# Kernel optimization log

Hardware: AMD Instinct MI355X
Metric: run time of the kernel (lower is better)

## Reference

```python
import jax, jax.numpy as jnp
import numpy as np
from jax import lax

D_MODEL = 1024
KERNEL = 7
EPS = 1e-8


def setup_inputs() -> dict:
    key = jax.random.key(0)
    ks = jax.random.split(key, 8)
    B, T, D = 4, 4096, D_MODEL
    x = jax.random.normal(ks[0], (B, T, D), dtype=jnp.float32)
    # rotary tables [T, D/2]
    pos = jnp.arange(T, dtype=jnp.float32)[:, None]
    inv_freq = 1.0 / (10000.0 ** (jnp.arange(D // 2, dtype=jnp.float32) / (D // 2)))
    ang = pos * inv_freq[None, :]
    sin = jnp.sin(ang)
    cos = jnp.cos(ang)
    # params
    W_proj = jax.random.normal(ks[1], (D, 2 * D), dtype=jnp.float32) * (1.0 / np.sqrt(D))
    b_proj = jnp.zeros((2 * D,), dtype=jnp.float32)
    dw_kernel = jax.random.normal(ks[2], (KERNEL, 1, D), dtype=jnp.float32) * 0.1  # [K,1,C] WIO depthwise
    dw_bias = jnp.zeros((D,), dtype=jnp.float32)
    gamma = jnp.ones((D,), dtype=jnp.float32)
    return {"x": x, "sin": sin, "cos": cos, "W_proj": W_proj, "b_proj": b_proj,
            "dw_kernel": dw_kernel, "dw_bias": dw_bias, "gamma": gamma}


def reference(x, sin, cos, W_proj, b_proj, dw_kernel, dw_bias, gamma):
    D = D_MODEL
    proj = jnp.einsum('btd,df->btf', x, W_proj) + b_proj          # [B,T,2D]
    x_a, x_b = proj[..., :D], proj[..., D:]
    # interleaved rotary: even/odd pairs
    x1 = x_a[..., 0::2]                                            # [B,T,D/2]
    x2 = x_a[..., 1::2]
    c = cos[None, :, :]
    s = sin[None, :, :]
    r1 = x1 * c - x2 * s
    r2 = x1 * s + x2 * c
    x_rot = jnp.stack([r1, r2], axis=-1).reshape(x_a.shape)        # re-interleave
    # depthwise conv1d, SAME padding
    conv = lax.conv_general_dilated(
        x_rot, dw_kernel, window_strides=(1,), padding='SAME',
        dimension_numbers=('NWC', 'WIO', 'NWC'), feature_group_count=D) + dw_bias
    act = conv * jax.nn.sigmoid(conv)                              # swish
    gated = act * jax.nn.sigmoid(x_b)
    rms = jnp.sqrt(jnp.mean(jnp.square(gated), axis=-1, keepdims=True) + EPS)
    return gamma * (gated / rms)
```

## Files before the change

kernel.cpp:

```cpp
#include <hip/hip_runtime.h>
#include <stdint.h>

#define D_MODEL 1024
#define T_LEN   4096
#define B_SZ    4
#define NROWS   (B_SZ * T_LEN)
#define NPROJ   (2 * D_MODEL)
#define CHUNK   16

#define BM 256
#define BN 256
#define BK 64
#define NT (D_MODEL / BK)

typedef __attribute__((ext_vector_type(8))) __bf16 bf16x8;
typedef __attribute__((ext_vector_type(4))) float  f32x4;

using as1_void = __attribute__((address_space(1))) void;
using as3_void = __attribute__((address_space(3))) void;

__device__ inline float bf2f(unsigned short u) {
    union { unsigned int i; float f; } v; v.i = ((unsigned int)u) << 16; return v.f;
}
__device__ inline unsigned short f2bf(float f) {
    union { float f; unsigned int i; } v; v.f = f;
    return (unsigned short)((v.i + 0x7fffu + ((v.i >> 16) & 1u)) >> 16);
}
__device__ inline float sigmoidf(float x) { return 1.0f / (1.0f + __expf(-x)); }

__global__ __launch_bounds__(256) void k_cvt(const float* __restrict__ x,
                                             unsigned short* __restrict__ xb,
                                             const float* __restrict__ W,
                                             unsigned short* __restrict__ wt) {
    __shared__ unsigned short tile[32][33];
    int bid = blockIdx.x;
    if (bid < (NROWS * D_MODEL) / (256 * 4)) {
        int i = (bid * 256 + threadIdx.x) * 4;
        float4 v = *reinterpret_cast<const float4*>(x + i);
        ushort4 o;
        o.x = f2bf(v.x); o.y = f2bf(v.y); o.z = f2bf(v.z); o.w = f2bf(v.w);
        *reinterpret_cast<ushort4*>(xb + i) = o;
    } else {
        bid -= (NROWS * D_MODEL) / (256 * 4);
        int n0 = (bid & 63) * 32, k0 = (bid >> 6) * 32;
        int c = threadIdx.x & 31, r = threadIdx.x >> 5;
        #pragma unroll
        for (int i = 0; i < 4; i++) {
            int kk = r + i * 8;
            tile[kk][c] = f2bf(W[(uint64_t)(k0 + kk) * NPROJ + n0 + c]);
        }
        __syncthreads();
        #pragma unroll
        for (int i = 0; i < 4; i++) {
            int nn = r + i * 8;
            wt[(uint64_t)(n0 + nn) * D_MODEL + k0 + c] = tile[c][nn];
        }
    }
}

__global__ __launch_bounds__(512, 2) void k_gemm(const unsigned short* __restrict__ xb,
                                                 const unsigned short* __restrict__ wt,
                                                 const float* __restrict__ bias,
                                                 unsigned short* __restrict__ projb) {
    __shared__ __align__(16) unsigned short As[2 * BM * BK];
    __shared__ __align__(16) unsigned short Bs[2 * BM * BK];

    const int tid  = threadIdx.x;
    const int lane = tid & 63;
    const int w    = tid >> 6;
    const int wm   = w >> 2;
    const int wn   = w & 3;

    const int bid = blockIdx.x;
    const int wg  = (bid & 7) * 64 + (bid >> 3);
    const int n0  = (wg >> 6) * BN;
    const int m0  = (wg & 63) * BM;

    const int srow = tid >> 3;
    const int scol = ((tid & 7) ^ (srow & 7)) * 8;
    const int fr   = lane & 15;
    const int fq   = lane >> 4;

    f32x4 acc[8][4] = {};

    auto STAGE = [&](int buf, int ks) {
        #pragma unroll
        for (int i = 0; i < 4; ++i) {
            const unsigned short* ga = xb + (uint64_t)(m0 + i * 64 + srow) * D_MODEL + ks + scol;
            __builtin_amdgcn_global_load_lds((as1_void*)(void*)ga,
                (as3_void*)(void*)&As[buf * (BM * BK) + i * 4096 + w * 512], 16, 0, 0);
        }
        #pragma unroll
        for (int i = 0; i < 4; ++i) {
            const unsigned short* gb = wt + (uint64_t)(n0 + i * 64 + srow) * D_MODEL + ks + scol;
            __builtin_amdgcn_global_load_lds((as1_void*)(void*)gb,
                (as3_void*)(void*)&Bs[buf * (BM * BK) + i * 4096 + w * 512], 16, 0, 0);
        }
    };

    STAGE(0, 0);
    __syncthreads();

    for (int t = 0; t < NT; ++t) {
        const int cur = t & 1;
        if (t + 1 < NT) STAGE(1 - cur, (t + 1) * BK);

        const unsigned short* Ab = &As[cur * (BM * BK)];
        const unsigned short* Bb = &Bs[cur * (BM * BK)];
        #pragma unroll
        for (int kk = 0; kk < BK; kk += 32) {
            const int slot = (kk >> 3) + fq;
            bf16x8 b[4];
            #pragma unroll
            for (int n = 0; n < 4; n++) {
                const int rb = wn * 64 + n * 16 + fr;
                b[n] = *reinterpret_cast<const bf16x8*>(&Bb[rb * 64 + ((slot ^ (fr & 7)) * 8)]);
            }
            #pragma unroll
            for (int m = 0; m < 8; m++) {
                const int ra = wm * 128 + m * 16 + fr;
                bf16x8 a = *reinterpret_cast<const bf16x8*>(&Ab[ra * 64 + ((slot ^ (fr & 7)) * 8)]);
                #pragma unroll
                for (int n = 0; n < 4; n++)
                    acc[m][n] = __builtin_amdgcn_mfma_f32_16x16x32_bf16(a, b[n], acc[m][n], 0, 0, 0);
            }
        }
        __syncthreads();
    }

    #pragma unroll
    for (int m = 0; m < 8; m++) {
        const int grow = m0 + wm * 128 + m * 16 + fq * 4;
        #pragma unroll
        for (int n = 0; n < 4; n++) {
            const int gcol = n0 + wn * 64 + n * 16 + fr;
            const float bv = bias[gcol];
            #pragma unroll
            for (int r = 0; r < 4; r++) {
                projb[(uint64_t)(grow + r) * NPROJ + gcol] = f2bf(acc[m][n][r] + bv);
            }
        }
    }
}

__global__ __launch_bounds__(512) void k_post(const unsigned short* __restrict__ projb,
                                              const float* __restrict__ kw,
                                              const float* __restrict__ dwb,
                                              const float* __restrict__ gamma,
                                              float* __restrict__ out) {
    const int blk  = blockIdx.x;
    const int b    = blk / (T_LEN / CHUNK);
    const int t0   = (blk % (T_LEN / CHUNK)) * CHUNK;
    const int c    = threadIdx.x;
    const int d0   = c * 2;
    const uint64_t bbase = (uint64_t)b * T_LEN;

    const float invf = exp2f((float)c * (-13.287712379549449f / 512.0f));

    float kwv[7][2];
    #pragma unroll
    for (int j = 0; j < 7; j++) {
        kwv[j][0] = kw[j * D_MODEL + d0];
        kwv[j][1] = kw[j * D_MODEL + d0 + 1];
    }
    const float bv0 = dwb[d0], bv1 = dwb[d0 + 1];
    const float gm0 = gamma[d0], gm1 = gamma[d0 + 1];

    __shared__ float partial[CHUNK][8];
    __shared__ float invr[CHUNK];

    auto load_rope = [&](int tj, float& o0, float& o1) {
        if ((unsigned)tj < (unsigned)T_LEN) {
            ushort2 u = *reinterpret_cast<const ushort2*>(projb + (bbase + tj) * NPROJ + d0);
            float sv, cv;
            __sincosf((float)tj * invf, &sv, &cv);
            float x0 = bf2f(u.x), x1 = bf2f(u.y);
            o0 = x0 * cv - x1 * sv;
            o1 = x0 * sv + x1 * cv;
        } else { o0 = 0.f; o1 = 0.f; }
    };

    float rg[6][2];
    #pragma unroll
    for (int j = 0; j < 6; j++) load_rope(t0 - 3 + j, rg[j][0], rg[j][1]);

    float ga[CHUNK], gb[CHUNK];

    #pragma unroll
    for (int r = 0; r < CHUNK; ++r) {
        float nx0, nx1;
        load_rope(t0 + r + 3, nx0, nx1);
        ushort2 xbv = *reinterpret_cast<const ushort2*>(
            projb + (bbase + t0 + r) * NPROJ + D_MODEL + d0);

        float acc0 = rg[0][0] * kwv[0][0] + rg[1][0] * kwv[1][0] + rg[2][0] * kwv[2][0]
                   + rg[3][0] * kwv[3][0] + rg[4][0] * kwv[4][0] + rg[5][0] * kwv[5][0]
                   + nx0 * kwv[6][0] + bv0;
        float acc1 = rg[0][1] * kwv[0][1] + rg[1][1] * kwv[1][1] + rg[2][1] * kwv[2][1]
                   + rg[3][1] * kwv[3][1] + rg[4][1] * kwv[4][1] + rg[5][1] * kwv[5][1]
                   + nx1 * kwv[6][1] + bv1;

        float a0 = acc0 * sigmoidf(acc0);
        float a1 = acc1 * sigmoidf(acc1);
        float g0 = a0 * sigmoidf(bf2f(xbv.x));
        float g1 = a1 * sigmoidf(bf2f(xbv.y));
        ga[r] = g0; gb[r] = g1;

        float ssq = g0 * g0 + g1 * g1;
        #pragma unroll
        for (int off = 32; off; off >>= 1) ssq += __shfl_down(ssq, off);
        if ((c & 63) == 0) partial[r][c >> 6] = ssq;

        #pragma unroll
        for (int j = 0; j < 5; j++) { rg[j][0] = rg[j + 1][0]; rg[j][1] = rg[j + 1][1]; }
        rg[5][0] = nx0; rg[5][1] = nx1;
    }

    __syncthreads();
    if (c < CHUNK) {
        float s = partial[c][0] + partial[c][1] + partial[c][2] + partial[c][3]
                + partial[c][4] + partial[c][5] + partial[c][6] + partial[c][7];
        invr[c] = 1.0f / sqrtf(s * (1.0f / (float)D_MODEL) + 1e-8f);
    }
    __syncthreads();

    #pragma unroll
    for (int r = 0; r < CHUNK; ++r) {
        const float iv = invr[r];
        float2 o;
        o.x = ga[r] * iv * gm0;
        o.y = gb[r] * iv * gm1;
        *reinterpret_cast<float2*>(out + (bbase + t0 + r) * D_MODEL + d0) = o;
    }
}

extern "C" void kernel_launch(void* const* d_in, const int* in_sizes, int n_in,
                              void* d_out, int out_size, void* d_ws, size_t ws_size,
                              hipStream_t stream) {
    const float* x     = (const float*)d_in[0];
    const float* sinp  = (const float*)d_in[1];
    const float* cosp  = (const float*)d_in[2];
    const float* W     = (const float*)d_in[3];
    const float* bproj = (const float*)d_in[4];
    const float* dwk   = (const float*)d_in[5];
    const float* dwb   = (const float*)d_in[6];
    const float* gamma = (const float*)d_in[7];
    float* out = (float*)d_out;
    (void)sinp; (void)cosp;

    unsigned short* xb    = (unsigned short*)d_ws;
    unsigned short* wt    = xb + (size_t)NROWS * D_MODEL;
    unsigned short* projb = wt + (size_t)NPROJ * D_MODEL;

    const int cvt_x_blocks = (NROWS * D_MODEL) / (256 * 4);
    const int cvt_w_blocks = (NPROJ / 32) * (D_MODEL / 32);
    k_cvt<<<cvt_x_blocks + cvt_w_blocks, 256, 0, stream>>>(x, xb, W, wt);
    k_gemm<<<(NPROJ / BN) * (NROWS / BM), 512, 0, stream>>>(xb, wt, bproj, projb);
    k_post<<<B_SZ * (T_LEN / CHUNK), 512, 0, stream>>>(projb, dwk, dwb, gamma, out);
}
```

Baseline: 147.6 us.

## Batch post-kernel loads, use recurrence for rotary angles, widen conversion stores

The post kernel now issues all conv-tap and gate loads up front (clamped addresses) before any computation, halves CHUNK to 8 to shrink per-thread register arrays and double the block count, and replaces per-row sincos calls with a rotation recurrence. The x conversion kernel handles 8 elements per thread with 16-byte stores. The goal is better memory-level parallelism in the post kernel and fewer transcendental ops. The cost is more redundant halo loads per chunk, and the recurrence may slowly lose precision across rows.

```diff
diff --git a/kernel.cpp b/kernel.cpp
--- a/kernel.cpp
+++ b/kernel.cpp
@@ -6,7 +6,7 @@
 #define B_SZ    4
 #define NROWS   (B_SZ * T_LEN)
 #define NPROJ   (2 * D_MODEL)
-#define CHUNK   16
+#define CHUNK   8
 
 #define BM 256
 #define BN 256
@@ -26,22 +26,30 @@
     union { float f; unsigned int i; } v; v.f = f;
     return (unsigned short)((v.i + 0x7fffu + ((v.i >> 16) & 1u)) >> 16);
 }
+__device__ inline unsigned int f2bf2(float lo, float hi) {
+    return (unsigned int)f2bf(lo) | ((unsigned int)f2bf(hi) << 16);
+}
 __device__ inline float sigmoidf(float x) { return 1.0f / (1.0f + __expf(-x)); }
 
+#define CVT_X_BLOCKS ((NROWS * D_MODEL) / (256 * 8))
 __global__ __launch_bounds__(256) void k_cvt(const float* __restrict__ x,
                                              unsigned short* __restrict__ xb,
                                              const float* __restrict__ W,
                                              unsigned short* __restrict__ wt) {
     __shared__ unsigned short tile[32][33];
     int bid = blockIdx.x;
-    if (bid < (NROWS * D_MODEL) / (256 * 4)) {
-        int i = (bid * 256 + threadIdx.x) * 4;
-        float4 v = *reinterpret_cast<const float4*>(x + i);
-        ushort4 o;
-        o.x = f2bf(v.x); o.y = f2bf(v.y); o.z = f2bf(v.z); o.w = f2bf(v.w);
-        *reinterpret_cast<ushort4*>(xb + i) = o;
+    if (bid < CVT_X_BLOCKS) {
+        int i = (bid * 256 + threadIdx.x) * 8;
+        float4 v0 = *reinterpret_cast<const float4*>(x + i);
+        float4 v1 = *reinterpret_cast<const float4*>(x + i + 4);
+        uint4 o;
+        o.x = f2bf2(v0.x, v0.y);
+        o.y = f2bf2(v0.z, v0.w);
+        o.z = f2bf2(v1.x, v1.y);
+        o.w = f2bf2(v1.z, v1.w);
+        *reinterpret_cast<uint4*>(xb + i) = o;
     } else {
-        bid -= (NROWS * D_MODEL) / (256 * 4);
+        bid -= CVT_X_BLOCKS;
         int n0 = (bid & 63) * 32, k0 = (bid >> 6) * 32;
         int c = threadIdx.x & 31, r = threadIdx.x >> 5;
         #pragma unroll
@@ -155,7 +163,23 @@
     const int d0   = c * 2;
     const uint64_t bbase = (uint64_t)b * T_LEN;
 
+    unsigned int tap[CHUNK + 7];
+    unsigned int xbv[CHUNK];
+    #pragma unroll
+    for (int i = 0; i < CHUNK + 7; ++i) {
+        int tj = t0 - 3 + i;
+        int ta = tj < 0 ? 0 : (tj >= T_LEN ? T_LEN - 1 : tj);
+        tap[i] = *reinterpret_cast<const unsigned int*>(projb + (bbase + ta) * NPROJ + d0);
+    }
+    #pragma unroll
+    for (int r = 0; r < CHUNK; ++r) {
+        xbv[r] = *reinterpret_cast<const unsigned int*>(projb + (bbase + t0 + r) * NPROJ + D_MODEL + d0);
+    }
+
     const float invf = exp2f((float)c * (-13.287712379549449f / 512.0f));
+    float sn, cs, sF, cF;
+    __sincosf((float)(t0 - 3) * invf, &sn, &cs);
+    __sincosf(invf, &sF, &cF);
 
     float kwv[7][2];
     #pragma unroll
@@ -169,51 +193,41 @@
     __shared__ float partial[CHUNK][8];
     __shared__ float invr[CHUNK];
 
-    auto load_rope = [&](int tj, float& o0, float& o1) {
-        if ((unsigned)tj < (unsigned)T_LEN) {
-            ushort2 u = *reinterpret_cast<const ushort2*>(projb + (bbase + tj) * NPROJ + d0);
-            float sv, cv;
-            __sincosf((float)tj * invf, &sv, &cv);
-            float x0 = bf2f(u.x), x1 = bf2f(u.y);
-            o0 = x0 * cv - x1 * sv;
-            o1 = x0 * sv + x1 * cv;
-        } else { o0 = 0.f; o1 = 0.f; }
-    };
-
-    float rg[6][2];
-    #pragma unroll
-    for (int j = 0; j < 6; j++) load_rope(t0 - 3 + j, rg[j][0], rg[j][1]);
+    float rx[CHUNK + 7][2];
+    #pragma unroll
+    for (int i = 0; i < CHUNK + 7; ++i) {
+        const int tj = t0 - 3 + i;
+        const bool valid = (unsigned)tj < (unsigned)T_LEN;
+        float x0 = bf2f((unsigned short)(tap[i] & 0xffffu));
+        float x1 = bf2f((unsigned short)(tap[i] >> 16));
+        float r0 = x0 * cs - x1 * sn;
+        float r1 = x0 * sn + x1 * cs;
+        rx[i][0] = valid ? r0 : 0.f;
+        rx[i][1] = valid ? r1 : 0.f;
+        float c2 = cs * cF - sn * sF;
+        sn = sn * cF + cs * sF;
+        cs = c2;
+    }
 
     float ga[CHUNK], gb[CHUNK];
-
     #pragma unroll
     for (int r = 0; r < CHUNK; ++r) {
-        float nx0, nx1;
-        load_rope(t0 + r + 3, nx0, nx1);
-        ushort2 xbv = *reinterpret_cast<const ushort2*>(
-            projb + (bbase + t0 + r) * NPROJ + D_MODEL + d0);
-
-        float acc0 = rg[0][0] * kwv[0][0] + rg[1][0] * kwv[1][0] + rg[2][0] * kwv[2][0]
-                   + rg[3][0] * kwv[3][0] + rg[4][0] * kwv[4][0] + rg[5][0] * kwv[5][0]
-                   + nx0 * kwv[6][0] + bv0;
-        float acc1 = rg[0][1] * kwv[0][1] + rg[1][1] * kwv[1][1] + rg[2][1] * kwv[2][1]
-                   + rg[3][1] * kwv[3][1] + rg[4][1] * kwv[4][1] + rg[5][1] * kwv[5][1]
-                   + nx1 * kwv[6][1] + bv1;
-
+        float acc0 = bv0, acc1 = bv1;
+        #pragma unroll
+        for (int j = 0; j < 7; j++) {
+            acc0 += rx[r + j][0] * kwv[j][0];
+            acc1 += rx[r + j][1] * kwv[j][1];
+        }
         float a0 = acc0 * sigmoidf(acc0);
         float a1 = acc1 * sigmoidf(acc1);
-        float g0 = a0 * sigmoidf(bf2f(xbv.x));
-        float g1 = a1 * sigmoidf(bf2f(xbv.y));
+        float g0 = a0 * sigmoidf(bf2f((unsigned short)(xbv[r] & 0xffffu)));
+        float g1 = a1 * sigmoidf(bf2f((unsigned short)(xbv[r] >> 16)));
         ga[r] = g0; gb[r] = g1;
 
         float ssq = g0 * g0 + g1 * g1;
         #pragma unroll
         for (int off = 32; off; off >>= 1) ssq += __shfl_down(ssq, off);
         if ((c & 63) == 0) partial[r][c >> 6] = ssq;
-
-        #pragma unroll
-        for (int j = 0; j < 5; j++) { rg[j][0] = rg[j + 1][0]; rg[j][1] = rg[j + 1][1]; }
-        rg[5][0] = nx0; rg[5][1] = nx1;
     }
 
     __syncthreads();
@@ -252,9 +266,8 @@
     unsigned short* wt    = xb + (size_t)NROWS * D_MODEL;
     unsigned short* projb = wt + (size_t)NPROJ * D_MODEL;
 
-    const int cvt_x_blocks = (NROWS * D_MODEL) / (256 * 4);
     const int cvt_w_blocks = (NPROJ / 32) * (D_MODEL / 32);
-    k_cvt<<<cvt_x_blocks + cvt_w_blocks, 256, 0, stream>>>(x, xb, W, wt);
+    k_cvt<<<CVT_X_BLOCKS + cvt_w_blocks, 256, 0, stream>>>(x, xb, W, wt);
     k_gemm<<<(NPROJ / BN) * (NROWS / BM), 512, 0, stream>>>(xb, wt, bproj, projb);
     k_post<<<B_SZ * (T_LEN / CHUNK), 512, 0, stream>>>(projb, dwk, dwb, gamma, out);
 }
```

New measurement: 135.3 us. 1.09x faster.
